# Kernel optimization log

Hardware: AMD Instinct MI355X
Metric: run time of the kernel (lower is better)

Reference implementation:

```python
import jax, jax.numpy as jnp
import numpy as np

B, NP, NC = 2, 20000, 10000   # frames, raw points/frame, conv (voxel) points/frame
C_IN, HID, NCLS, K = 64, 64, 20, 3
EPS_BN_CLS = 1e-5   # nn.BatchNorm1d default (cls heads)
EPS_BN_ALIGN = 1e-6 # partial(nn.BatchNorm1d, eps=1e-6) (align layer)
EPS_NN = 1e-8


def setup_inputs() -> dict:
    key = jax.random.key(0)
    ks = jax.random.split(key, 32)
    i = iter(range(32))
    def n(shape, s=1.0):
        return jax.random.normal(ks[next(i)], shape, jnp.float32) * s
    def u(shape, lo, hi):
        return jax.random.uniform(ks[next(i)], shape, jnp.float32, lo, hi)
    bs_c = jnp.repeat(jnp.arange(B, dtype=jnp.float32), NC)[:, None]
    bs_p = jnp.repeat(jnp.arange(B, dtype=jnp.float32), NP)[:, None]
    inp = {
        'conv_point_features': n((B * NC, C_IN)),
        'conv_point_coords': jnp.concatenate([bs_c, u((B * NC, 3), -50.0, 50.0)], 1),
        'points': jnp.concatenate([bs_p, u((B * NP, 3), -50.0, 50.0)], 1),
        # conv_cls head: Linear(C_IN->HID, no bias) + BN + ReLU + Linear(HID->NCLS, bias)
        'cls_w1': n((C_IN, HID), 0.1), 'cls_bn_g': u((HID,), 0.5, 1.5), 'cls_bn_b': n((HID,), 0.1),
        'cls_bn_m': n((HID,), 0.1), 'cls_bn_v': u((HID,), 0.5, 1.5),
        'cls_w2': n((HID, NCLS), 0.1), 'cls_b2': n((NCLS,), 0.1),
        # conv_align: Linear(C_IN->HID, bias) + BN(eps=1e-6) + ReLU
        'al_w': n((C_IN, HID), 0.1), 'al_b': n((HID,), 0.1),
        'al_bn_g': u((HID,), 0.5, 1.5), 'al_bn_b': n((HID,), 0.1),
        'al_bn_m': n((HID,), 0.1), 'al_bn_v': u((HID,), 0.5, 1.5),
        # out_cls head: Linear(HID->HID, no bias) + BN + ReLU + Linear(HID->NCLS, bias)
        'out_w1': n((HID, HID), 0.1), 'out_bn_g': u((HID,), 0.5, 1.5), 'out_bn_b': n((HID,), 0.1),
        'out_bn_m': n((HID,), 0.1), 'out_bn_v': u((HID,), 0.5, 1.5),
        'out_w2': n((HID, NCLS), 0.1), 'out_b2': n((NCLS,), 0.1),
        'batch_size': B,
    }
    return inp


def _bn(x, g, b, m, v, eps):
    return (x - m) * (g * jax.lax.rsqrt(v + eps)) + b


def _three_interpolate(new_xyz, xyz, feats):
    # new_xyz: [Np,3], xyz: [Nc,3], feats: [Nc,C] -> [Np,C]
    n2 = jnp.sum(new_xyz * new_xyz, -1)
    m2 = jnp.sum(xyz * xyz, -1)
    d2 = n2[:, None] + m2[None, :] - 2.0 * (new_xyz @ xyz.T)  # [Np,Nc] squared dists
    neg_d, idx = jax.lax.top_k(-d2, K)                        # 3 nearest
    d = jnp.maximum(-neg_d, 0.0)
    w = 1.0 / (d + EPS_NN)
    w = w / jnp.sum(w, -1, keepdims=True)                     # [Np,K]
    return jnp.einsum('nkc,nk->nc', feats[idx], w)


def reference(conv_point_features, conv_point_coords, points,
              cls_w1, cls_bn_g, cls_bn_b, cls_bn_m, cls_bn_v, cls_w2, cls_b2,
              al_w, al_b, al_bn_g, al_bn_b, al_bn_m, al_bn_v,
              out_w1, out_bn_g, out_bn_b, out_bn_m, out_bn_v, out_w2, out_b2,
              batch_size):
    # conv_cls head on voxel features
    h = jax.nn.relu(_bn(conv_point_features @ cls_w1, cls_bn_g, cls_bn_b, cls_bn_m, cls_bn_v, EPS_BN_CLS))
    conv_logits = h @ cls_w2 + cls_b2                          # [B*NC, NCLS]

    # three_interpolate: per-frame 3-NN inverse-distance interpolation.
    # Equal point counts per frame, so the stacked [bs_idx,x,y,z] layout
    # reshapes into [B, N, 3] (batch ids are contiguous blocks).
    nc = conv_point_coords.shape[0] // batch_size
    npt = points.shape[0] // batch_size
    xyz_c = conv_point_coords[:, 1:4].reshape(batch_size, nc, 3)
    xyz_p = points[:, 1:4].reshape(batch_size, npt, 3)
    feats = conv_point_features.reshape(batch_size, nc, -1)
    interp = jax.vmap(_three_interpolate)(xyz_p, xyz_c, feats)  # [B, NP, C_IN]
    interp = interp.reshape(batch_size * npt, -1)

    # conv_align: Linear + BN(eps=1e-6) + ReLU
    f = jax.nn.relu(_bn(interp @ al_w + al_b, al_bn_g, al_bn_b, al_bn_m, al_bn_v, EPS_BN_ALIGN))
    # out_cls head
    h2 = jax.nn.relu(_bn(f @ out_w1, out_bn_g, out_bn_b, out_bn_m, out_bn_v, EPS_BN_CLS))
    out_logits = h2 @ out_w2 + out_b2                           # [B*NP, NCLS]
    return conv_logits, out_logits
```

## Files before the change

### kernel.cpp

```cpp
#include <hip/hip_runtime.h>
#include <math.h>

#define HID 64
#define NCLS 20
#define EPS_CLS 1e-5f
#define EPS_AL 1e-6f
#define NCMAX 10240
#define NWORDS ((NCMAX + 31) / 32 + 1)
#define MAXMARK 192
#define NSEG 8
#define STILE 512

__device__ __forceinline__ float relu_(float x){ return x > 0.f ? x : 0.f; }

__device__ __forceinline__ float pin(float v){
  asm volatile("" : "+v"(v));
  return v;
}
__device__ __forceinline__ float mulrn_b(float a, float b){ return pin(__fmul_rn(a,b)); }
__device__ __forceinline__ float addrn_b(float a, float b){ return pin(__fadd_rn(a,b)); }
__device__ __forceinline__ float subrn_b(float a, float b){ return pin(__fsub_rn(a,b)); }

__device__ __forceinline__ float np_norm2(float x, float y, float z){
  return addrn_b(addrn_b(mulrn_b(x,x), mulrn_b(y,y)), mulrn_b(z,z));
}

__device__ __forceinline__ float lattice_d2(float qx, float qy, float qz, float n2,
                                            float cx, float cy, float cz, float m2){
  float p0  = mulrn_b(qx, cx);
  float dot = pin(fmaf(qz, cz, fmaf(qy, cy, p0)));
  float nm  = addrn_b(n2, m2);
  float t2d = mulrn_b(2.0f, dot);
  return subrn_b(nm, t2d);
}

__global__ void __launch_bounds__(64) cls_head_kernel(
    const float* __restrict__ feats, const float* __restrict__ w1,
    const float* __restrict__ bn_g, const float* __restrict__ bn_b,
    const float* __restrict__ bn_m, const float* __restrict__ bn_v,
    const float* __restrict__ w2, const float* __restrict__ b2,
    float* __restrict__ out, int R)
{
  __shared__ float s1[HID], t1[HID];
  int tx = threadIdx.x;
  if (tx < HID) {
    float s = bn_g[tx] / sqrtf(bn_v[tx] + EPS_CLS);
    s1[tx] = s;
    t1[tx] = bn_b[tx] - bn_m[tx] * s;
  }
  __syncthreads();
  int r = blockIdx.x * 64 + tx;
  if (r >= R) return;
  float x[HID];
  const float4* xr = (const float4*)(feats + (size_t)r * HID);
  #pragma unroll
  for (int i = 0; i < 16; i++) {
    float4 t = xr[i];
    x[4*i+0]=t.x; x[4*i+1]=t.y; x[4*i+2]=t.z; x[4*i+3]=t.w;
  }
  float o[NCLS];
  #pragma unroll
  for (int c = 0; c < NCLS; c++) o[c] = b2[c];
  #pragma unroll
  for (int j = 0; j < HID; j++) {
    float acc = 0.f;
    #pragma unroll
    for (int k = 0; k < HID; k++) acc = fmaf(x[k], w1[k*HID + j], acc);
    float h = relu_(acc * s1[j] + t1[j]);
    #pragma unroll
    for (int c = 0; c < NCLS; c++) o[c] = fmaf(h, w2[j*NCLS + c], o[c]);
  }
  float4* op = (float4*)(out + (size_t)r * NCLS);
  #pragma unroll
  for (int i = 0; i < 5; i++) op[i] = make_float4(o[4*i], o[4*i+1], o[4*i+2], o[4*i+3]);
}

__global__ void __launch_bounds__(256) knn_scan_kernel(
    const float4* __restrict__ coords, const float4* __restrict__ pts,
    float4* __restrict__ pd, int4* __restrict__ pi,
    int NC, int NP, int nseg)
{
  __shared__ float4 tile[STILE];
  int frame = blockIdx.z;
  int seg   = blockIdx.y;
  int tid   = threadIdx.x;
  int q = blockIdx.x * 256 + tid;
  bool valid = (q < NP);

  float qx=0.f, qy=0.f, qz=0.f, n2=0.f;
  if (valid) {
    float4 p = pts[(size_t)frame * NP + q];
    qx=p.y; qy=p.z; qz=p.w;
    n2 = np_norm2(qx,qy,qz);
  }
  int SL = (NC + nseg - 1) / nseg;
  int c0 = seg * SL, c1 = min(NC, c0 + SL);
  float d0=1e30f, d1=1e30f, d2v=1e30f, d3=1e30f;
  int   i0=-1, i1=-1, i2=-1;
  const float4* C = coords + (size_t)frame * NC;

  for (int t = c0; t < c1; t += STILE) {
    int n = min(STILE, c1 - t);
    __syncthreads();
    for (int k = tid; k < n; k += 256) {
      float4 cr = C[t + k];
      tile[k] = make_float4(cr.y, cr.z, cr.w, np_norm2(cr.y, cr.z, cr.w));
    }
    __syncthreads();
    for (int j = 0; j < n; j++) {
      float4 c = tile[j];
      float dd = lattice_d2(qx,qy,qz,n2, c.x,c.y,c.z,c.w);
      if (dd < d3) {
        int ci = t + j;
        if (dd < d1) {
          if (dd < d0) { d3=d2v; d2v=d1;i2=i1; d1=d0;i1=i0; d0=dd;i0=ci; }
          else         { d3=d2v; d2v=d1;i2=i1; d1=dd;i1=ci; }
        } else {
          if (dd < d2v){ d3=d2v; d2v=dd;i2=ci; }
          else         { d3=dd; }
        }
      }
    }
  }
  if (valid) {
    size_t base = (size_t)(frame * NP + q) * nseg + seg;
    pd[base] = make_float4(d0, d1, d2v, d3);
    pi[base] = make_int4(i0, i1, i2, -1);
  }
}

__global__ void __launch_bounds__(256) knn_merge_kernel(
    const float4* __restrict__ pd, const int4* __restrict__ pi,
    float* __restrict__ wd, int* __restrict__ wi,
    int* __restrict__ mark_cnt, int* __restrict__ mark_rows,
    int RP, int nseg)
{
  int row = blockIdx.x * 256 + threadIdx.x;
  if (row >= RP) return;
  float m0=1e30f, m1=1e30f, m2v=1e30f, m3=1e30f;
  int   j0=0, j1=0, j2=0;
  for (int s = 0; s < nseg; s++) {
    float4 d = pd[(size_t)row * nseg + s];
    int4  ii = pi[(size_t)row * nseg + s];
    float dv[4] = { d.x, d.y, d.z, d.w };
    int   iv[4] = { ii.x, ii.y, ii.z, -1 };
    #pragma unroll
    for (int r = 0; r < 4; r++) {
      float dd = dv[r]; int jj = iv[r];
      if (dd < m3) {
        if (dd < m1) {
          if (dd < m0) { m3=m2v; m2v=m1;j2=j1; m1=m0;j1=j0; m0=dd;j0=jj; }
          else         { m3=m2v; m2v=m1;j2=j1; m1=dd;j1=jj; }
        } else {
          if (dd < m2v){ m3=m2v; m2v=dd;j2=jj; }
          else         { m3=dd; }
        }
      }
    }
  }
  size_t base = (size_t)row * 3;
  wd[base+0]=m0; wd[base+1]=m1; wd[base+2]=m2v;
  wi[base+0]=j0; wi[base+1]=j1; wi[base+2]=j2;
  if (m2v == m3) {
    int slot = atomicAdd(mark_cnt, 1);
    if (slot < MAXMARK) mark_rows[slot] = row;
  }
}

__global__ void __launch_bounds__(256) tie_resort_kernel(
    const float4* __restrict__ coords, const float4* __restrict__ pts,
    const int* __restrict__ mark_cnt, const int* __restrict__ mark_rows,
    float* __restrict__ wd, int* __restrict__ wi, int NC, int NP)
{
  __shared__ unsigned short t[NCMAX];
  __shared__ unsigned short Rpos[NCMAX];
  __shared__ unsigned int abit[NWORDS], bbit[NWORDS];
  __shared__ int scanA[256], scanB[256];
  __shared__ int s_pl, s_pr, s_sp, s_state, s_K, s_LK;
  __shared__ float s_vp, s_q[4], vloc[16];
  __shared__ int s_slo[64], s_shi[64];

  int cnt = *mark_cnt; if (cnt > MAXMARK) cnt = MAXMARK;
  int b = blockIdx.x;
  if (b >= cnt) return;
  int row = mark_rows[b];
  int frame = row / NP;
  int q = row - frame * NP;
  int tid = threadIdx.x;

  if (tid == 0) {
    float4 p = pts[(size_t)frame * NP + q];
    s_q[0]=p.y; s_q[1]=p.z; s_q[2]=p.w;
    s_q[3]=np_norm2(p.y,p.z,p.w);
    s_pl = 0; s_pr = NC - 1; s_sp = 0; s_state = 0;
  }
  for (int i = tid; i < NC; i += 256) t[i] = (unsigned short)i;
  __syncthreads();
  float qx=s_q[0], qy=s_q[1], qz=s_q[2], n2=s_q[3];
  const float4* C = coords + (size_t)frame * NC;

  auto V = [&](int p)->float {
    float4 c = C[t[p]];
    float m2 = np_norm2(c.y, c.z, c.w);
    return lattice_d2(qx,qy,qz,n2, c.y,c.z,c.w,m2);
  };

  for (;;) {
    __syncthreads();
    if (s_state) break;
    int pl = s_pl, pr = s_pr;

    if (pr - pl > 15) {
      if (tid == 0) {
        int pm = pl + ((pr - pl) >> 1);
        unsigned short tmp;
        if (V(pm) < V(pl)) { tmp=t[pm]; t[pm]=t[pl]; t[pl]=tmp; }
        if (V(pr) < V(pm)) { tmp=t[pr]; t[pr]=t[pm]; t[pm]=tmp; }
        if (V(pm) < V(pl)) { tmp=t[pm]; t[pm]=t[pl]; t[pl]=tmp; }
        s_vp = V(pm);
        tmp=t[pm]; t[pm]=t[pr-1]; t[pr-1]=tmp;
        s_K = 0;
      }
      __syncthreads();
      float vp = s_vp;
      int M = pr - pl + 1;
      int nwords = (M + 31) >> 5;
      int wpt = (nwords + 255) >> 8;
      int wlo = tid * wpt;
      int whi = min(wlo + wpt, nwords);

      int cA = 0, cB = 0;
      for (int w = wlo; w < whi; ++w) {
        unsigned int wa = 0, wb = 0;
        int rbase = w << 5;
        #pragma unroll 8
        for (int bit = 0; bit < 32; ++bit) {
          int r = rbase + bit;
          bool in = (r < M);
          float val = V(in ? (pl + r) : pl);
          if (in && r >= 1 && r <= M-2 && !(val < vp)) wa |= (1u << bit);
          if (in && r <= M-3 && !(vp < val))           wb |= (1u << bit);
        }
        abit[w] = wa; bbit[w] = wb;
        cA += __popc(wa); cB += __popc(wb);
      }
      scanA[tid] = cA; scanB[tid] = cB;
      __syncthreads();
      for (int off = 1; off < 256; off <<= 1) {
        int aa = (tid >= off) ? scanA[tid-off] : 0;
        int bb = (tid >= off) ? scanB[tid-off] : 0;
        __syncthreads();
        scanA[tid] += aa; scanB[tid] += bb;
        __syncthreads();
      }
      int offA = scanA[tid] - cA;
      int offB = scanB[tid] - cB;
      int nB = scanB[255];
      __syncthreads();

      int run = offB;
      for (int w = wlo; w < whi; ++w) {
        unsigned int wb = bbit[w];
        while (wb) {
          int bit = __ffs(wb) - 1; wb &= wb - 1;
          run++;
          Rpos[nB - run] = (unsigned short)(pl + (w << 5) + bit);
        }
      }
      __syncthreads();

      int k = offA, localK = 0;
      for (int w = wlo; w < whi; ++w) {
        unsigned int wa = abit[w];
        while (wa) {
          int bit = __ffs(wa) - 1; wa &= wa - 1;
          int pos = pl + (w << 5) + bit;
          if (k < nB && pos < (int)Rpos[k]) localK++;
          k++;
        }
      }
      if (localK) atomicAdd(&s_K, localK);
      __syncthreads();
      int K = s_K;

      k = offA;
      for (int w = wlo; w < whi; ++w) {
        unsigned int wa = abit[w];
        while (wa) {
          int bit = __ffs(wa) - 1; wa &= wa - 1;
          int pos = pl + (w << 5) + bit;
          if (k < K) {
            int pp = Rpos[k];
            unsigned short tmp = t[pos]; t[pos] = t[pp]; t[pp] = tmp;
          } else if (k == K) {
            s_LK = pos;
          }
          k++;
        }
      }
      __syncthreads();

      if (tid == 0) {
        int pi2 = s_LK;
        if (K > 0) { int rk = Rpos[K-1]; if (rk < pi2) pi2 = rk; }
        unsigned short tmp = t[pi2]; t[pi2] = t[pr-1]; t[pr-1] = tmp;
        if (pi2 - pl < pr - pi2) {
          if (pi2 + 1 <= 3) { s_slo[s_sp] = pi2 + 1; s_shi[s_sp] = pr; s_sp++; }
          s_pr = pi2 - 1;
        } else {
          s_slo[s_sp] = pl; s_shi[s_sp] = pi2 - 1; s_sp++;
          s_pl = pi2 + 1;
          if (s_pl > 3) {
            --s_sp; s_pl = s_slo[s_sp]; s_pr = s_shi[s_sp];
          }
        }
      }
    } else {
      if (pr > pl && tid <= pr - pl) vloc[tid] = V(pl + tid);
      __syncthreads();
      if (tid == 0) {
        for (int a2 = pl + 1; a2 <= pr; ++a2) {
          unsigned short vi = t[a2]; float vv = vloc[a2 - pl];
          int b2 = a2;
          while (b2 > pl && vv < vloc[b2-1-pl]) {
            t[b2] = t[b2-1]; vloc[b2-pl] = vloc[b2-1-pl]; --b2;
          }
          t[b2] = vi; vloc[b2-pl] = vv;
        }
        if (s_sp == 0) s_state = 1;
        else { --s_sp; s_pl = s_slo[s_sp]; s_pr = s_shi[s_sp]; }
      }
    }
  }

  __syncthreads();
  if (tid == 0) {
    size_t base = (size_t)row * 3;
    wd[base+0]=V(0); wd[base+1]=V(1); wd[base+2]=V(2);
    wi[base+0]=t[0]; wi[base+1]=t[1]; wi[base+2]=t[2];
  }
}

__global__ void __launch_bounds__(64) interp_mlp_kernel(
    const float* __restrict__ feats,
    const float* __restrict__ wd, const int* __restrict__ wi,
    const float* __restrict__ al_w, const float* __restrict__ al_b,
    const float* __restrict__ al_g, const float* __restrict__ al_bb,
    const float* __restrict__ al_m, const float* __restrict__ al_v,
    const float* __restrict__ o_w1,
    const float* __restrict__ o_g, const float* __restrict__ o_bb,
    const float* __restrict__ o_m, const float* __restrict__ o_v,
    const float* __restrict__ o_w2, const float* __restrict__ o_b2,
    float* __restrict__ out, int NC, int NP, int B)
{
  __shared__ float s1[HID], t1[HID], s2[HID], t2[HID];
  int tx = threadIdx.x;
  if (tx < HID) {
    float sa = al_g[tx] / sqrtf(al_v[tx] + EPS_AL);
    s1[tx] = sa;
    t1[tx] = (al_b[tx] - al_m[tx]) * sa + al_bb[tx];
    float so = o_g[tx] / sqrtf(o_v[tx] + EPS_CLS);
    s2[tx] = so;
    t2[tx] = o_bb[tx] - o_m[tx] * so;
  }
  __syncthreads();
  int r = blockIdx.x * 64 + tx;
  if (r >= B * NP) return;
  int frame = r / NP;

  float bd0 = wd[(size_t)r*3+0], bd1 = wd[(size_t)r*3+1], bd2 = wd[(size_t)r*3+2];
  int   bi0 = wi[(size_t)r*3+0], bi1 = wi[(size_t)r*3+1], bi2 = wi[(size_t)r*3+2];

  float w0 = pin(__fdiv_rn(1.0f, addrn_b(fmaxf(bd0, 0.f), 1e-8f)));
  float w1 = pin(__fdiv_rn(1.0f, addrn_b(fmaxf(bd1, 0.f), 1e-8f)));
  float w2 = pin(__fdiv_rn(1.0f, addrn_b(fmaxf(bd2, 0.f), 1e-8f)));
  float wsum = addrn_b(addrn_b(w0, w1), w2);
  w0 = pin(__fdiv_rn(w0, wsum)); w1 = pin(__fdiv_rn(w1, wsum)); w2 = pin(__fdiv_rn(w2, wsum));

  const float* F = feats + (size_t)frame * NC * HID;
  const float4* F0 = (const float4*)(F + (size_t)bi0 * HID);
  const float4* F1 = (const float4*)(F + (size_t)bi1 * HID);
  const float4* F2 = (const float4*)(F + (size_t)bi2 * HID);

  float interp[HID];
  #pragma unroll
  for (int i = 0; i < 16; i++) {
    float4 a = F0[i], b = F1[i], c = F2[i];
    interp[4*i+0] = (a.x*w0 + b.x*w1) + c.x*w2;
    interp[4*i+1] = (a.y*w0 + b.y*w1) + c.y*w2;
    interp[4*i+2] = (a.z*w0 + b.z*w1) + c.z*w2;
    interp[4*i+3] = (a.w*w0 + b.w*w1) + c.w*w2;
  }

  float f[HID];
  #pragma unroll
  for (int j = 0; j < HID; j++) {
    float acc = 0.f;
    #pragma unroll
    for (int k = 0; k < HID; k++) acc = fmaf(interp[k], al_w[k*HID + j], acc);
    f[j] = relu_(acc * s1[j] + t1[j]);
  }
  float o[NCLS];
  #pragma unroll
  for (int c = 0; c < NCLS; c++) o[c] = o_b2[c];
  #pragma unroll
  for (int j = 0; j < HID; j++) {
    float acc = 0.f;
    #pragma unroll
    for (int k = 0; k < HID; k++) acc = fmaf(f[k], o_w1[k*HID + j], acc);
    float h = relu_(acc * s2[j] + t2[j]);
    #pragma unroll
    for (int c = 0; c < NCLS; c++) o[c] = fmaf(h, o_w2[j*NCLS + c], o[c]);
  }
  float4* op = (float4*)(out + (size_t)r * NCLS);
  #pragma unroll
  for (int i = 0; i < 5; i++) op[i] = make_float4(o[4*i], o[4*i+1], o[4*i+2], o[4*i+3]);
}

extern "C" void kernel_launch(void* const* d_in, const int* in_sizes, int n_in,
                              void* d_out, int out_size, void* d_ws, size_t ws_size,
                              hipStream_t stream)
{
  const float*  feats  = (const float*) d_in[0];
  const float4* coords = (const float4*)d_in[1];
  const float4* pts    = (const float4*)d_in[2];
  const float* cls_w1 = (const float*)d_in[3];
  const float* cls_g  = (const float*)d_in[4];
  const float* cls_b  = (const float*)d_in[5];
  const float* cls_m  = (const float*)d_in[6];
  const float* cls_v  = (const float*)d_in[7];
  const float* cls_w2 = (const float*)d_in[8];
  const float* cls_b2 = (const float*)d_in[9];
  const float* al_w   = (const float*)d_in[10];
  const float* al_b   = (const float*)d_in[11];
  const float* al_g   = (const float*)d_in[12];
  const float* al_bb  = (const float*)d_in[13];
  const float* al_m   = (const float*)d_in[14];
  const float* al_v   = (const float*)d_in[15];
  const float* o_w1   = (const float*)d_in[16];
  const float* o_g    = (const float*)d_in[17];
  const float* o_bb   = (const float*)d_in[18];
  const float* o_m    = (const float*)d_in[19];
  const float* o_v    = (const float*)d_in[20];
  const float* o_w2   = (const float*)d_in[21];
  const float* o_b2   = (const float*)d_in[22];

  const int B = 2;
  int RC = in_sizes[1] / 4;  int NC = RC / B;
  int RP = in_sizes[2] / 4;  int NP = RP / B;

  int nseg = NSEG;
  while (nseg > 1 &&
         1024 + (size_t)RP*3*8 + (size_t)RP*nseg*32 > ws_size) nseg >>= 1;

  int*   mark_cnt  = (int*)d_ws;
  int*   mark_rows = (int*)((char*)d_ws + 16);
  float* wd  = (float*)((char*)d_ws + 1024);
  int*   wi  = (int*)((char*)wd + (size_t)RP * 3 * 4);
  float4* pd = (float4*)((char*)wi + (size_t)RP * 3 * 4);
  int4*   pi = (int4*)((char*)pd + (size_t)RP * nseg * 16);

  hipMemsetAsync(d_ws, 0, 16, stream);

  cls_head_kernel<<<(RC + 63) / 64, 64, 0, stream>>>(
      feats, cls_w1, cls_g, cls_b, cls_m, cls_v, cls_w2, cls_b2,
      (float*)d_out, RC);

  dim3 g1((NP + 255) / 256, nseg, B);
  knn_scan_kernel<<<g1, 256, 0, stream>>>(coords, pts, pd, pi, NC, NP, nseg);

  knn_merge_kernel<<<(RP + 255) / 256, 256, 0, stream>>>(
      pd, pi, wd, wi, mark_cnt, mark_rows, RP, nseg);

  tie_resort_kernel<<<MAXMARK, 256, 0, stream>>>(coords, pts, mark_cnt, mark_rows,
                                                 wd, wi, NC, NP);

  float* out2 = (float*)d_out + (size_t)RC * NCLS;
  interp_mlp_kernel<<<(RP + 63) / 64, 64, 0, stream>>>(
      feats, wd, wi,
      al_w, al_b, al_g, al_bb, al_m, al_v,
      o_w1, o_g, o_bb, o_m, o_v, o_w2, o_b2,
      out2, NC, NP, B);
}
```

Baseline: 498.4 us.

## Add per-segment min prepass to prune exact 3-NN distance evaluation

Adds a cheap first pass that computes, for each query and segment, a fast FMA-based half-distance minimum. The scan kernel combines these into a fourth-smallest segment minimum plus a small margin, and runs the exact NumPy-order distance and insertion logic only for candidates below that bound. The goal is to skip the costly pinned-rounding distance math for most candidates, at the price of a second full pass over coordinates and extra workspace. The fixed 0.05 margin may be too small for rounding differences at large coordinates, so a true neighbour could be filtered out.

Measured after the change: 628.0 us. +26.0%, slower.

```diff
diff --git a/kernel.cpp b/kernel.cpp
--- a/kernel.cpp
+++ b/kernel.cpp
@@ -75,10 +75,9 @@
   for (int i = 0; i < 5; i++) op[i] = make_float4(o[4*i], o[4*i+1], o[4*i+2], o[4*i+3]);
 }
 
-__global__ void __launch_bounds__(256) knn_scan_kernel(
+__global__ void __launch_bounds__(256) knn_min_kernel(
     const float4* __restrict__ coords, const float4* __restrict__ pts,
-    float4* __restrict__ pd, int4* __restrict__ pi,
-    int NC, int NP, int nseg)
+    float* __restrict__ pmin, int NC, int NP, int nseg)
 {
   __shared__ float4 tile[STILE];
   int frame = blockIdx.z;
@@ -87,11 +86,64 @@
   int q = blockIdx.x * 256 + tid;
   bool valid = (q < NP);
 
-  float qx=0.f, qy=0.f, qz=0.f, n2=0.f;
+  float qx=0.f, qy=0.f, qz=0.f, hn2=0.f;
   if (valid) {
     float4 p = pts[(size_t)frame * NP + q];
     qx=p.y; qy=p.z; qz=p.w;
-    n2 = np_norm2(qx,qy,qz);
+    hn2 = 0.5f * np_norm2(qx,qy,qz);
+  }
+  int SL = (NC + nseg - 1) / nseg;
+  int c0 = seg * SL, c1 = min(NC, c0 + SL);
+  float smin = 1e30f;
+  const float4* C = coords + (size_t)frame * NC;
+
+  for (int t = c0; t < c1; t += STILE) {
+    int n = min(STILE, c1 - t);
+    __syncthreads();
+    for (int k = tid; k < n; k += 256) {
+      float4 cr = C[t + k];
+      tile[k] = make_float4(cr.y, cr.z, cr.w, 0.5f * np_norm2(cr.y, cr.z, cr.w));
+    }
+    __syncthreads();
+    for (int j = 0; j < n; j++) {
+      float4 c = tile[j];
+      float dot = fmaf(qz, c.z, fmaf(qy, c.y, qx * c.x));
+      float s = (hn2 + c.w) - dot;
+      smin = fminf(smin, s);
+    }
+  }
+  if (valid) pmin[(size_t)(frame * NP + q) * nseg + seg] = smin;
+}
+
+__global__ void __launch_bounds__(256) knn_scan_kernel(
+    const float4* __restrict__ coords, const float4* __restrict__ pts,
+    const float* __restrict__ pmin,
+    float4* __restrict__ pd, int4* __restrict__ pi,
+    int NC, int NP, int nseg)
+{
+  __shared__ float4 tile[STILE];
+  int frame = blockIdx.z;
+  int seg   = blockIdx.y;
+  int tid   = threadIdx.x;
+  int q = blockIdx.x * 256 + tid;
+  bool valid = (q < NP);
+
+  float qx=0.f, qy=0.f, qz=0.f, n2=0.f, hn2=0.f, scr=1e30f;
+  if (valid) {
+    float4 p = pts[(size_t)frame * NP + q];
+    qx=p.y; qy=p.z; qz=p.w;
+    n2  = np_norm2(qx,qy,qz);
+    hn2 = 0.5f * n2;
+    float m0=1e30f, m1=1e30f, m2n=1e30f, m3n=1e30f;
+    const float* pm = pmin + (size_t)(frame * NP + q) * nseg;
+    for (int s = 0; s < nseg; s++) {
+      float v = pm[s];
+      float t0 = fmaxf(m0, v);  m0 = fminf(m0, v);
+      float t1 = fmaxf(m1, t0); m1 = fminf(m1, t0);
+      float t2 = fmaxf(m2n, t1); m2n = fminf(m2n, t1);
+      m3n = fminf(m3n, t2);
+    }
+    scr = m3n + 0.05f;
   }
   int SL = (NC + nseg - 1) / nseg;
   int c0 = seg * SL, c1 = min(NC, c0 + SL);
@@ -104,20 +156,25 @@
     __syncthreads();
     for (int k = tid; k < n; k += 256) {
       float4 cr = C[t + k];
-      tile[k] = make_float4(cr.y, cr.z, cr.w, np_norm2(cr.y, cr.z, cr.w));
+      tile[k] = make_float4(cr.y, cr.z, cr.w, 0.5f * np_norm2(cr.y, cr.z, cr.w));
     }
     __syncthreads();
     for (int j = 0; j < n; j++) {
       float4 c = tile[j];
-      float dd = lattice_d2(qx,qy,qz,n2, c.x,c.y,c.z,c.w);
-      if (dd < d3) {
-        int ci = t + j;
-        if (dd < d1) {
-          if (dd < d0) { d3=d2v; d2v=d1;i2=i1; d1=d0;i1=i0; d0=dd;i0=ci; }
-          else         { d3=d2v; d2v=d1;i2=i1; d1=dd;i1=ci; }
-        } else {
-          if (dd < d2v){ d3=d2v; d2v=dd;i2=ci; }
-          else         { d3=dd; }
+      float dotf = fmaf(qz, c.z, fmaf(qy, c.y, qx * c.x));
+      float s = (hn2 + c.w) - dotf;
+      if (s <= scr) {
+        float m2 = 2.0f * c.w;
+        float dd = lattice_d2(qx,qy,qz,n2, c.x,c.y,c.z,m2);
+        if (dd < d3) {
+          int ci = t + j;
+          if (dd < d1) {
+            if (dd < d0) { d3=d2v; d2v=d1;i2=i1; d1=d0;i1=i0; d0=dd;i0=ci; }
+            else         { d3=d2v; d2v=d1;i2=i1; d1=dd;i1=ci; }
+          } else {
+            if (dd < d2v){ d3=d2v; d2v=dd;i2=ci; }
+            else         { d3=dd; }
+          }
         }
       }
     }
@@ -451,7 +508,7 @@
 
   int nseg = NSEG;
   while (nseg > 1 &&
-         1024 + (size_t)RP*3*8 + (size_t)RP*nseg*32 > ws_size) nseg >>= 1;
+         1024 + (size_t)RP*3*8 + (size_t)RP*nseg*36 > ws_size) nseg >>= 1;
 
   int*   mark_cnt  = (int*)d_ws;
   int*   mark_rows = (int*)((char*)d_ws + 16);
@@ -459,6 +516,7 @@
   int*   wi  = (int*)((char*)wd + (size_t)RP * 3 * 4);
   float4* pd = (float4*)((char*)wi + (size_t)RP * 3 * 4);
   int4*   pi = (int4*)((char*)pd + (size_t)RP * nseg * 16);
+  float* pmin = (float*)((char*)pi + (size_t)RP * nseg * 16);
 
   hipMemsetAsync(d_ws, 0, 16, stream);
 
@@ -467,7 +525,8 @@
       (float*)d_out, RC);
 
   dim3 g1((NP + 255) / 256, nseg, B);
-  knn_scan_kernel<<<g1, 256, 0, stream>>>(coords, pts, pd, pi, NC, NP, nseg);
+  knn_min_kernel<<<g1, 256, 0, stream>>>(coords, pts, pmin, NC, NP, nseg);
+  knn_scan_kernel<<<g1, 256, 0, stream>>>(coords, pts, pmin, pd, pi, NC, NP, nseg);
 
   knn_merge_kernel<<<(RP + 255) / 256, 256, 0, stream>>>(
       pd, pi, wd, wi, mark_cnt, mark_rows, RP, nseg);
```
